# Performance work log

Hardware: AMD Instinct MI355X
Metric: run time of the kernel (lower is better)

## Reference

```python
import jax, jax.numpy as jnp
import numpy as np

NEG_SLOPE = 0.2


def gat_layer(x, W, a_src, a_dst, b, src, dst, num_nodes, heads, out_c, concat):
    # Linear transform per head: [N, heads, out_c]
    h = (x @ W).reshape(num_nodes, heads, out_c)
    # Per-node attention logits for source/dest roles: [N, heads]
    e_src = jnp.einsum('nhc,hc->nh', h, a_src)
    e_dst = jnp.einsum('nhc,hc->nh', h, a_dst)
    # Edge-wise scores (gather), LeakyReLU: [E, heads]
    e = jax.nn.leaky_relu(e_src[src] + e_dst[dst], negative_slope=NEG_SLOPE)
    # Segment softmax over incoming edges of each destination node
    m = jax.ops.segment_max(e, dst, num_segments=num_nodes)
    ex = jnp.exp(e - m[dst])
    denom = jax.ops.segment_sum(ex, dst, num_segments=num_nodes)
    alpha = ex / denom[dst]                       # [E, heads]
    # Weighted scatter-aggregate of source messages: [N, heads, out_c]
    out = jax.ops.segment_sum(h[src] * alpha[:, :, None], dst, num_segments=num_nodes)
    if concat:
        out = out.reshape(num_nodes, heads * out_c)
    else:
        out = out.mean(axis=1)
    return out + b


def setup_inputs() -> dict:
    key = jax.random.key(0)
    ks = jax.random.split(key, 12)
    N, E = 50000, 800000
    in_c, out_c, heads = 128, 32, 4
    x = jax.random.normal(ks[0], (N, in_c), dtype=jnp.float32)
    edge_index = jax.random.randint(ks[1], (2, E), 0, N, dtype=jnp.int64)
    s1 = 1.0 / np.sqrt(in_c)
    W1 = jax.random.normal(ks[2], (in_c, heads * out_c), dtype=jnp.float32) * s1
    a_src1 = jax.random.normal(ks[3], (heads, out_c), dtype=jnp.float32) * 0.1
    a_dst1 = jax.random.normal(ks[4], (heads, out_c), dtype=jnp.float32) * 0.1
    b1 = jnp.zeros((heads * out_c,), dtype=jnp.float32)
    s2 = 1.0 / np.sqrt(heads * out_c)
    W2 = jax.random.normal(ks[5], (heads * out_c, out_c), dtype=jnp.float32) * s2
    a_src2 = jax.random.normal(ks[6], (1, out_c), dtype=jnp.float32) * 0.1
    a_dst2 = jax.random.normal(ks[7], (1, out_c), dtype=jnp.float32) * 0.1
    b2 = jnp.zeros((out_c,), dtype=jnp.float32)
    return {"x": x, "edge_index": edge_index, "W1": W1, "a_src1": a_src1,
            "a_dst1": a_dst1, "b1": b1, "W2": W2, "a_src2": a_src2,
            "a_dst2": a_dst2, "b2": b2}


def reference(x, edge_index, W1, a_src1, a_dst1, b1, W2, a_src2, a_dst2, b2):
    N = x.shape[0]
    heads, out_c = a_src1.shape
    # add_self_loops=True (PyG default)
    loops = jnp.arange(N, dtype=edge_index.dtype)
    src = jnp.concatenate([edge_index[0], loops])
    dst = jnp.concatenate([edge_index[1], loops])
    h1 = gat_layer(x, W1, a_src1, a_dst1, b1, src, dst, N, heads, out_c, concat=True)
    h1 = jax.nn.elu(h1)
    out = gat_layer(h1, W2, a_src2, a_dst2, b2, src, dst, N, 1, out_c, concat=False)
    return out
```

## Files before the change

kernel.cpp:

```cpp
#include <hip/hip_runtime.h>
#include <hip/hip_bf16.h>

#define LRELU_SLOPE 0.2f
#define NB_SHIFT 7
#define NBLK 512

typedef __attribute__((ext_vector_type(8))) short short8;
typedef __attribute__((ext_vector_type(4))) float float4v;

__device__ inline float b2f(unsigned short u) {
    union { unsigned int i; float f; } v; v.i = ((unsigned int)u) << 16; return v.f;
}
__device__ inline unsigned short f2b(float f) {
    union { float f; unsigned int i; } v; v.f = f;
    unsigned int x = v.i;
    unsigned int r = x + 0x7fffu + ((x >> 16) & 1u);
    return (unsigned short)(r >> 16);
}
__device__ inline float lrelu(float x) { return x > 0.f ? x : LRELU_SLOPE * x; }

__global__ __launch_bounds__(256) void gemm1_mfma_kernel(
        const float* __restrict__ x, const float* __restrict__ W1,
        const float* __restrict__ a_src, const float* __restrict__ a_dst,
        unsigned short* __restrict__ h1b, float* __restrict__ es,
        float* __restrict__ ed, int N,
        const int* __restrict__ dst, int E, int Etot, int nb, int chunk,
        int* __restrict__ cnt) {
    __shared__ unsigned short xs[64][136];
    __shared__ unsigned short wt[128][136];
    int tid = threadIdx.x;
    int n0 = blockIdx.x * 64;

    for (int i = tid; i < 128 * 128; i += 256) {
        int k = i >> 7, n = i & 127;
        wt[n][k] = f2b(W1[i]);
    }
    for (int i = tid; i < 64 * 128; i += 256) {
        int r = i >> 7, k = i & 127;
        int row = n0 + r; if (row >= N) row = N - 1;
        xs[r][k] = f2b(x[(size_t)row * 128 + k]);
    }
    __syncthreads();

    int wave = tid >> 6;
    int lane = tid & 63;
    int lrow = lane & 15;
    int quad = lane >> 4;

    short8 afr[4];
#pragma unroll
    for (int kc = 0; kc < 4; kc++)
        afr[kc] = *(const short8*)&xs[wave * 16 + lrow][kc * 32 + quad * 8];
    __syncthreads();

#pragma unroll
    for (int ct = 0; ct < 8; ct++) {
        float4v acc = {0.f, 0.f, 0.f, 0.f};
#pragma unroll
        for (int kc = 0; kc < 4; kc++) {
            short8 bfr = *(const short8*)&wt[ct * 16 + lrow][kc * 32 + quad * 8];
            acc = __builtin_amdgcn_mfma_f32_16x16x32_bf16(afr[kc], bfr, acc, 0, 0, 0);
        }
#pragma unroll
        for (int r = 0; r < 4; r++) {
            int lr = wave * 16 + quad * 4 + r;
            int grow = n0 + lr;
            unsigned short hb = f2b(acc[r]);
            xs[lr][ct * 16 + lrow] = hb;
            if (grow < N)
                h1b[grow * 128 + ct * 16 + lrow] = hb;
        }
    }
    __syncthreads();

    int row = tid >> 2, h = tid & 3;
    int rg = n0 + row;
    if (rg < N) {
        const float* ap = a_src + h * 32;
        const float* bp = a_dst + h * 32;
        float s = 0.f, d = 0.f;
#pragma unroll
        for (int c2 = 0; c2 < 16; c2++) {
            unsigned int u = *(const unsigned int*)&xs[row][h * 32 + 2 * c2];
            float v0 = b2f((unsigned short)(u & 0xffffu));
            float v1 = b2f((unsigned short)(u >> 16));
            float2 a = *(const float2*)&ap[2 * c2];
            float2 b = *(const float2*)&bp[2 * c2];
            s += v0 * a.x + v1 * a.y;
            d += v0 * b.x + v1 * b.y;
        }
        es[rg * 4 + h] = s;
        ed[rg * 4 + h] = d;
    }

    int* histm = (int*)&wt[0][0];
    int blk = blockIdx.x;
    if (blk < NBLK)
        for (int i = tid; i < nb; i += 256) histm[i] = 0;
    __syncthreads();
    if (blk < NBLK) {
        int lo = blk * chunk;
        int hi = lo + chunk; if (hi > Etot) hi = Etot;
        for (int i = lo + tid; i < hi; i += 256) {
            int d = (i < E) ? dst[i] : (i - E);
            atomicAdd(&histm[d >> NB_SHIFT], 1);
        }
    }
    __syncthreads();
    if (blk < NBLK)
        for (int b = tid; b < nb; b += 256)
            cnt[b * NBLK + blk] = histm[b];
}

__global__ __launch_bounds__(1024) void scanA_kernel(int* cnt, int* bsum, int M) {
    __shared__ int tile[1024];
    int i = blockIdx.x * 1024 + threadIdx.x;
    int v = (i < M) ? cnt[i] : 0;
    tile[threadIdx.x] = v;
    __syncthreads();
    for (int off = 1; off < 1024; off <<= 1) {
        int t = (threadIdx.x >= (unsigned)off) ? tile[threadIdx.x - off] : 0;
        __syncthreads();
        tile[threadIdx.x] += t;
        __syncthreads();
    }
    int incl = tile[threadIdx.x];
    if (i < M) cnt[i] = incl - v;
    if (threadIdx.x == 1023) bsum[blockIdx.x] = incl;
}

__global__ __launch_bounds__(256) void scanB_kernel(int* __restrict__ bsum, int nb) {
    __shared__ int tile[256];
    int v = (threadIdx.x < (unsigned)nb) ? bsum[threadIdx.x] : 0;
    tile[threadIdx.x] = v;
    __syncthreads();
    for (int off = 1; off < 256; off <<= 1) {
        int t = (threadIdx.x >= (unsigned)off) ? tile[threadIdx.x - off] : 0;
        __syncthreads();
        tile[threadIdx.x] += t;
        __syncthreads();
    }
    if (threadIdx.x < (unsigned)nb) bsum[threadIdx.x] = tile[threadIdx.x] - v;
}

__global__ __launch_bounds__(256) void partition_kernel(
        const int* __restrict__ src, const int* __restrict__ dst,
        int E, int Etot, int nb, int chunk,
        const int* __restrict__ cnt, const int* __restrict__ boff,
        int2* __restrict__ bkt) {
    __shared__ int cur[512];
    int blk = blockIdx.x;
    for (int b = threadIdx.x; b < nb; b += 256) {
        int idx = b * NBLK + blk;
        cur[b] = cnt[idx] + boff[idx >> 10];
    }
    __syncthreads();
    int lo = blk * chunk;
    int hi = lo + chunk; if (hi > Etot) hi = Etot;
    for (int i = lo + threadIdx.x; i < hi; i += 256) {
        int s, d;
        if (i < E) { s = src[i]; d = dst[i]; }
        else       { s = d = i - E; }
        int pos = atomicAdd(&cur[d >> NB_SHIFT], 1);
        bkt[pos] = make_int2(s, d);
    }
}

__global__ __launch_bounds__(256) void finalize_kernel(
        const int2* __restrict__ bkt, const int* __restrict__ cnt,
        const int* __restrict__ boff, int nb,
        const float* __restrict__ es, const float* __restrict__ ed,
        int* __restrict__ ptr, int* __restrict__ csr_src,
        _Float16* __restrict__ w1h, int N, int Etot) {
    __shared__ int deg[128];
    __shared__ int scn[128];
    __shared__ int cur[128];
    int b = blockIdx.x;
    int idx0 = b * NBLK;
    int base = cnt[idx0] + boff[idx0 >> 10];
    int nextbase;
    if (b + 1 < nb) {
        int idx1 = (b + 1) * NBLK;
        nextbase = cnt[idx1] + boff[idx1 >> 10];
    } else nextbase = Etot;
    int count = nextbase - base;
    int node0 = b << NB_SHIFT;
    int nodes = N - node0; if (nodes > 128) nodes = 128;

    if (threadIdx.x < 128) deg[threadIdx.x] = 0;
    __syncthreads();
    for (int i = threadIdx.x; i < count; i += 256)
        atomicAdd(&deg[bkt[base + i].y - node0], 1);
    __syncthreads();
    int v = (threadIdx.x < 128) ? deg[threadIdx.x] : 0;
    if (threadIdx.x < 128) scn[threadIdx.x] = v;
    __syncthreads();
    for (int off = 1; off < 128; off <<= 1) {
        int t = (threadIdx.x < 128 && threadIdx.x >= (unsigned)off) ? scn[threadIdx.x - off] : 0;
        __syncthreads();
        if (threadIdx.x < 128) scn[threadIdx.x] += t;
        __syncthreads();
    }
    if (threadIdx.x < 128) {
        int excl = scn[threadIdx.x] - v;
        cur[threadIdx.x] = excl;
        if (threadIdx.x < nodes) ptr[node0 + threadIdx.x] = base + excl;
    }
    if (b == nb - 1 && threadIdx.x == 0) ptr[N] = Etot;
    __syncthreads();
    for (int i = threadIdx.x; i < count; i += 256) {
        int2 sd = bkt[base + i];
        int pos = base + atomicAdd(&cur[sd.y - node0], 1);
        csr_src[pos] = sd.x;
        float4 a = *(const float4*)&es[sd.x * 4];
        float4 bb = *(const float4*)&ed[sd.y * 4];
        union { _Float16 h[4]; uint2 u; } ww;
        ww.h[0] = (_Float16)__expf(lrelu(a.x + bb.x));
        ww.h[1] = (_Float16)__expf(lrelu(a.y + bb.y));
        ww.h[2] = (_Float16)__expf(lrelu(a.z + bb.z));
        ww.h[3] = (_Float16)__expf(lrelu(a.w + bb.w));
        *(uint2*)&w1h[(size_t)pos * 4] = ww.u;
    }
}

__global__ __launch_bounds__(256) void gemm2_mfma_kernel(
        const unsigned short* __restrict__ h1e, const float* __restrict__ W2,
        const float* __restrict__ a_src, const float* __restrict__ a_dst,
        unsigned short* __restrict__ h2b, float* __restrict__ es,
        float* __restrict__ ed, int N) {
    __shared__ unsigned short xs[64][136];
    __shared__ unsigned short wt[32][136];
    int tid = threadIdx.x;
    int n0 = blockIdx.x * 64;

    for (int i = tid; i < 128 * 32; i += 256) {
        int k = i >> 5, n = i & 31;
        wt[n][k] = f2b(W2[i]);
    }
    {
        const unsigned int* srcp = (const unsigned int*)(h1e + (size_t)n0 * 128);
        int rows = (N - n0) < 64 ? (N - n0) : 64;
        int maxu = rows * 64;
        for (int i = tid; i < 4096; i += 256) {
            unsigned int v = (i < maxu) ? srcp[i] : 0u;
            int r = i >> 6, cp = (i & 63) << 1;
            *(unsigned int*)&xs[r][cp] = v;
        }
    }
    __syncthreads();

    int wave = tid >> 6;
    int lane = tid & 63;
    int lrow = lane & 15;
    int quad = lane >> 4;

    short8 afr[4];
#pragma unroll
    for (int kc = 0; kc < 4; kc++)
        afr[kc] = *(const short8*)&xs[wave * 16 + lrow][kc * 32 + quad * 8];
    __syncthreads();

#pragma unroll
    for (int ct = 0; ct < 2; ct++) {
        float4v acc = {0.f, 0.f, 0.f, 0.f};
#pragma unroll
        for (int kc = 0; kc < 4; kc++) {
            short8 bfr = *(const short8*)&wt[ct * 16 + lrow][kc * 32 + quad * 8];
            acc = __builtin_amdgcn_mfma_f32_16x16x32_bf16(afr[kc], bfr, acc, 0, 0, 0);
        }
#pragma unroll
        for (int r = 0; r < 4; r++) {
            int lr = wave * 16 + quad * 4 + r;
            int grow = n0 + lr;
            unsigned short hb = f2b(acc[r]);
            xs[lr][ct * 16 + lrow] = hb;
            if (grow < N)
                h2b[(size_t)grow * 32 + ct * 16 + lrow] = hb;
        }
    }
    __syncthreads();

    if (tid < 64) {
        int rg = n0 + tid;
        if (rg < N) {
            float s = 0.f, d = 0.f;
#pragma unroll
            for (int c2 = 0; c2 < 16; c2++) {
                unsigned int u = *(const unsigned int*)&xs[tid][2 * c2];
                float v0 = b2f((unsigned short)(u & 0xffffu));
                float v1 = b2f((unsigned short)(u >> 16));
                float2 a = *(const float2*)&a_src[2 * c2];
                float2 b = *(const float2*)&a_dst[2 * c2];
                s += v0 * a.x + v1 * a.y;
                d += v0 * b.x + v1 * b.y;
            }
            es[rg] = s;
            ed[rg] = d;
        }
    }
}

__global__ __launch_bounds__(256) void agg1_kernel(
        const uint4* __restrict__ h1v, const _Float16* __restrict__ w1h,
        const int* __restrict__ csr, const int* __restrict__ ptr,
        const float* __restrict__ b1, uint4* __restrict__ h1e_v, int N) {
    int tid = threadIdx.x;
    int n = blockIdx.x * 16 + (tid >> 4);
    if (n >= N) return;
    int cl = tid & 15;
    int h = cl >> 2;
    int start = ptr[n], end = ptr[n + 1];
    float a0 = 0.f, a1 = 0.f, a2 = 0.f, a3 = 0.f;
    float a4 = 0.f, a5 = 0.f, a6 = 0.f, a7 = 0.f, ws = 0.f;
    int i = start;
    for (; i + 4 <= end; i += 4) {
        int s[4]; float v[4]; uint4 g[4];
#pragma unroll
        for (int k = 0; k < 4; k++) s[k] = csr[i + k];
#pragma unroll
        for (int k = 0; k < 4; k++) v[k] = (float)w1h[(size_t)(i + k) * 4 + h];
#pragma unroll
        for (int k = 0; k < 4; k++) g[k] = h1v[(s[k] << 4) + cl];
#pragma unroll
        for (int k = 0; k < 4; k++) {
            a0 += v[k] * b2f((unsigned short)(g[k].x & 0xffffu));
            a1 += v[k] * b2f((unsigned short)(g[k].x >> 16));
            a2 += v[k] * b2f((unsigned short)(g[k].y & 0xffffu));
            a3 += v[k] * b2f((unsigned short)(g[k].y >> 16));
            a4 += v[k] * b2f((unsigned short)(g[k].z & 0xffffu));
            a5 += v[k] * b2f((unsigned short)(g[k].z >> 16));
            a6 += v[k] * b2f((unsigned short)(g[k].w & 0xffffu));
            a7 += v[k] * b2f((unsigned short)(g[k].w >> 16));
            ws += v[k];
        }
    }
    for (; i < end; i++) {
        int s = csr[i];
        float v = (float)w1h[(size_t)i * 4 + h];
        uint4 g = h1v[(s << 4) + cl];
        a0 += v * b2f((unsigned short)(g.x & 0xffffu));
        a1 += v * b2f((unsigned short)(g.x >> 16));
        a2 += v * b2f((unsigned short)(g.y & 0xffffu));
        a3 += v * b2f((unsigned short)(g.y >> 16));
        a4 += v * b2f((unsigned short)(g.z & 0xffffu));
        a5 += v * b2f((unsigned short)(g.z >> 16));
        a6 += v * b2f((unsigned short)(g.w & 0xffffu));
        a7 += v * b2f((unsigned short)(g.w >> 16));
        ws += v;
    }
    float r = 1.f / ws;
    float4 bb0 = ((const float4*)b1)[cl * 2];
    float4 bb1 = ((const float4*)b1)[cl * 2 + 1];
    float o0 = a0 * r + bb0.x;
    float o1 = a1 * r + bb0.y;
    float o2 = a2 * r + bb0.z;
    float o3 = a3 * r + bb0.w;
    float o4 = a4 * r + bb1.x;
    float o5 = a5 * r + bb1.y;
    float o6 = a6 * r + bb1.z;
    float o7 = a7 * r + bb1.w;
    o0 = o0 > 0.f ? o0 : __expf(o0) - 1.f;
    o1 = o1 > 0.f ? o1 : __expf(o1) - 1.f;
    o2 = o2 > 0.f ? o2 : __expf(o2) - 1.f;
    o3 = o3 > 0.f ? o3 : __expf(o3) - 1.f;
    o4 = o4 > 0.f ? o4 : __expf(o4) - 1.f;
    o5 = o5 > 0.f ? o5 : __expf(o5) - 1.f;
    o6 = o6 > 0.f ? o6 : __expf(o6) - 1.f;
    o7 = o7 > 0.f ? o7 : __expf(o7) - 1.f;
    uint4 outv;
    outv.x = (unsigned int)f2b(o0) | ((unsigned int)f2b(o1) << 16);
    outv.y = (unsigned int)f2b(o2) | ((unsigned int)f2b(o3) << 16);
    outv.z = (unsigned int)f2b(o4) | ((unsigned int)f2b(o5) << 16);
    outv.w = (unsigned int)f2b(o6) | ((unsigned int)f2b(o7) << 16);
    h1e_v[(n << 4) + cl] = outv;
}

__global__ __launch_bounds__(256) void agg2_kernel(
        const uint2* __restrict__ h2v, const float* __restrict__ es,
        const float* __restrict__ ed, const int* __restrict__ csr,
        const int* __restrict__ ptr, const float* __restrict__ b2,
        float* __restrict__ out, int N) {
    int tid = threadIdx.x;
    int n = blockIdx.x * 32 + (tid >> 3);
    if (n >= N) return;
    int cl = tid & 7;
    float edl = ed[n];
    int start = ptr[n], end = ptr[n + 1];
    float a0 = 0.f, a1 = 0.f, a2 = 0.f, a3 = 0.f, ws = 0.f;
    int i = start;
    for (; i + 8 <= end; i += 8) {
        int s[8]; float e[8]; uint2 g[8];
#pragma unroll
        for (int k = 0; k < 8; k++) s[k] = csr[i + k];
#pragma unroll
        for (int k = 0; k < 8; k++) e[k] = es[s[k]];
#pragma unroll
        for (int k = 0; k < 8; k++) g[k] = h2v[(s[k] << 3) + cl];
#pragma unroll
        for (int k = 0; k < 8; k++) {
            float v = __expf(lrelu(e[k] + edl));
            a0 += v * b2f((unsigned short)(g[k].x & 0xffffu));
            a1 += v * b2f((unsigned short)(g[k].x >> 16));
            a2 += v * b2f((unsigned short)(g[k].y & 0xffffu));
            a3 += v * b2f((unsigned short)(g[k].y >> 16));
            ws += v;
        }
    }
    for (; i < end; i++) {
        int s = csr[i];
        float v = __expf(lrelu(es[s] + edl));
        uint2 g = h2v[(s << 3) + cl];
        a0 += v * b2f((unsigned short)(g.x & 0xffffu));
        a1 += v * b2f((unsigned short)(g.x >> 16));
        a2 += v * b2f((unsigned short)(g.y & 0xffffu));
        a3 += v * b2f((unsigned short)(g.y >> 16));
        ws += v;
    }
    float r = 1.f / ws;
    float4 bb = ((const float4*)b2)[cl];
    float4 o;
    o.x = a0 * r + bb.x;
    o.y = a1 * r + bb.y;
    o.z = a2 * r + bb.z;
    o.w = a3 * r + bb.w;
    ((float4*)out)[(size_t)n * 8 + cl] = o;
}

extern "C" void kernel_launch(void* const* d_in, const int* in_sizes, int n_in,
                              void* d_out, int out_size, void* d_ws, size_t ws_size,
                              hipStream_t stream) {
    const float* x      = (const float*)d_in[0];
    const int*   ei     = (const int*)  d_in[1];
    const float* W1     = (const float*)d_in[2];
    const float* a_src1 = (const float*)d_in[3];
    const float* a_dst1 = (const float*)d_in[4];
    const float* b1     = (const float*)d_in[5];
    const float* W2     = (const float*)d_in[6];
    const float* a_src2 = (const float*)d_in[7];
    const float* a_dst2 = (const float*)d_in[8];
    const float* b2     = (const float*)d_in[9];
    float* outp = (float*)d_out;

    const int N = in_sizes[0] / 128;
    const int E = in_sizes[1] / 2;
    const int Etot = E + N;

    const int* src = ei;
    const int* dst = ei + E;

    const int nb    = (N + 127) >> 7;
    const int chunk = (Etot + NBLK - 1) / NBLK;
    const int M = nb * NBLK;
    const int nbA = (M + 1023) / 1024;

    char* w = (char*)d_ws;
    unsigned short* h1b = (unsigned short*)(w + 0);
    unsigned short* h1e = (unsigned short*)(w + 12800000);
    unsigned short* h2b = (unsigned short*)(w + 25600000);
    float* es1  = (float*)(w + 28800000);
    float* ed1  = (float*)(w + 29600000);
    float* es2  = (float*)(w + 30400000);
    float* ed2  = (float*)(w + 30600000);
    int*   ptr  = (int*)  (w + 30800000);
    int*   bsum = (int*)  (w + 31000064);
    int*   cnt  = (int*)  (w + 31001088);
    int*   csr_src = (int*)(w + 31801856);
    int2*  bkt  = (int2*) (w + 35201856);
    _Float16* w1h = (_Float16*)(w + 42001856);

    gemm1_mfma_kernel<<<(N + 63) / 64, 256, 0, stream>>>(x, W1, a_src1, a_dst1,
                                                         h1b, es1, ed1, N,
                                                         dst, E, Etot, nb, chunk, cnt);

    scanA_kernel<<<nbA, 1024, 0, stream>>>(cnt, bsum, M);
    scanB_kernel<<<1, 256, 0, stream>>>(bsum, nbA);
    partition_kernel<<<NBLK, 256, 0, stream>>>(src, dst, E, Etot, nb, chunk,
                                               cnt, bsum, bkt);
    finalize_kernel<<<nb, 256, 0, stream>>>(bkt, cnt, bsum, nb, es1, ed1,
                                            ptr, csr_src, w1h, N, Etot);

    agg1_kernel<<<(N + 15) / 16, 256, 0, stream>>>((const uint4*)h1b, w1h,
                                                   csr_src, ptr, b1,
                                                   (uint4*)h1e, N);

    gemm2_mfma_kernel<<<(N + 63) / 64, 256, 0, stream>>>(h1e, W2, a_src2, a_dst2,
                                                         h2b, es2, ed2, N);
    agg2_kernel<<<(N + 31) / 32, 256, 0, stream>>>((const uint2*)h2b, es2, ed2,
                                                   csr_src, ptr, b2, outp, N);
}
```

Before: 198.6 us.

## Fuse scan kernels, recompute edge weights in aggregation, vectorize x load, halve partition blocks

Merges the two-level scan into one kernel, where the last block to finish (tracked by an atomic counter that gemm1 resets) scans the block sums. Edge attention weights are no longer precomputed and stored as fp16 in finalize. agg1 now gathers es per source and recomputes exp(leaky_relu) inline, which removes a per-edge buffer write and read at the cost of an extra gather and exp per lane. The x tile load in gemm1 becomes float4-vectorized, and the partition block count drops from 512 to 256, shrinking the count matrix and scan.

```diff
diff --git a/kernel.cpp b/kernel.cpp
--- a/kernel.cpp
+++ b/kernel.cpp
@@ -3,7 +3,7 @@
 
 #define LRELU_SLOPE 0.2f
 #define NB_SHIFT 7
-#define NBLK 512
+#define NBLK 256
 
 typedef __attribute__((ext_vector_type(8))) short short8;
 typedef __attribute__((ext_vector_type(4))) float float4v;
@@ -25,20 +25,29 @@
         unsigned short* __restrict__ h1b, float* __restrict__ es,
         float* __restrict__ ed, int N,
         const int* __restrict__ dst, int E, int Etot, int nb, int chunk,
-        int* __restrict__ cnt) {
+        int* __restrict__ cnt, int* __restrict__ done_ctr) {
     __shared__ unsigned short xs[64][136];
     __shared__ unsigned short wt[128][136];
     int tid = threadIdx.x;
     int n0 = blockIdx.x * 64;
+    if (blockIdx.x == 0 && tid == 0) done_ctr[0] = 0;
 
     for (int i = tid; i < 128 * 128; i += 256) {
         int k = i >> 7, n = i & 127;
         wt[n][k] = f2b(W1[i]);
     }
-    for (int i = tid; i < 64 * 128; i += 256) {
-        int r = i >> 7, k = i & 127;
-        int row = n0 + r; if (row >= N) row = N - 1;
-        xs[r][k] = f2b(x[(size_t)row * 128 + k]);
+    {
+        int rows = N - n0; if (rows > 64) rows = 64;
+        const float4* xv = (const float4*)(x + (size_t)n0 * 128);
+        int lim = rows * 32;
+        for (int i = tid; i < lim; i += 256) {
+            float4 v = xv[i];
+            int r = i >> 5, c4 = (i & 31) << 2;
+            uint2 p;
+            p.x = (unsigned int)f2b(v.x) | ((unsigned int)f2b(v.y) << 16);
+            p.y = (unsigned int)f2b(v.z) | ((unsigned int)f2b(v.w) << 16);
+            *(uint2*)&xs[r][c4] = p;
+        }
     }
     __syncthreads();
 
@@ -112,8 +121,10 @@
             cnt[b * NBLK + blk] = histm[b];
 }
 
-__global__ __launch_bounds__(1024) void scanA_kernel(int* cnt, int* bsum, int M) {
+__global__ __launch_bounds__(1024) void scanAB_kernel(int* cnt, int* bsum, int M,
+                                                      int nbA, int* done_ctr) {
     __shared__ int tile[1024];
+    __shared__ int amLast;
     int i = blockIdx.x * 1024 + threadIdx.x;
     int v = (i < M) ? cnt[i] : 0;
     tile[threadIdx.x] = v;
@@ -127,20 +138,22 @@
     int incl = tile[threadIdx.x];
     if (i < M) cnt[i] = incl - v;
     if (threadIdx.x == 1023) bsum[blockIdx.x] = incl;
-}
-
-__global__ __launch_bounds__(256) void scanB_kernel(int* __restrict__ bsum, int nb) {
-    __shared__ int tile[256];
-    int v = (threadIdx.x < (unsigned)nb) ? bsum[threadIdx.x] : 0;
-    tile[threadIdx.x] = v;
-    __syncthreads();
-    for (int off = 1; off < 256; off <<= 1) {
-        int t = (threadIdx.x >= (unsigned)off) ? tile[threadIdx.x - off] : 0;
+    __threadfence();
+    if (threadIdx.x == 0)
+        amLast = (atomicAdd(done_ctr, 1) == (int)gridDim.x - 1);
+    __syncthreads();
+    if (amLast) {
+        int vv = (threadIdx.x < (unsigned)nbA) ? bsum[threadIdx.x] : 0;
+        tile[threadIdx.x] = vv;
         __syncthreads();
-        tile[threadIdx.x] += t;
-        __syncthreads();
-    }
-    if (threadIdx.x < (unsigned)nb) bsum[threadIdx.x] = tile[threadIdx.x] - v;
+        for (int off = 1; off < 1024; off <<= 1) {
+            int t = (threadIdx.x >= (unsigned)off) ? tile[threadIdx.x - off] : 0;
+            __syncthreads();
+            tile[threadIdx.x] += t;
+            __syncthreads();
+        }
+        if (threadIdx.x < (unsigned)nbA) bsum[threadIdx.x] = tile[threadIdx.x] - vv;
+    }
 }
 
 __global__ __launch_bounds__(256) void partition_kernel(
@@ -169,9 +182,7 @@
 __global__ __launch_bounds__(256) void finalize_kernel(
         const int2* __restrict__ bkt, const int* __restrict__ cnt,
         const int* __restrict__ boff, int nb,
-        const float* __restrict__ es, const float* __restrict__ ed,
-        int* __restrict__ ptr, int* __restrict__ csr_src,
-        _Float16* __restrict__ w1h, int N, int Etot) {
+        int* __restrict__ ptr, int* __restrict__ csr_src, int N, int Etot) {
     __shared__ int deg[128];
     __shared__ int scn[128];
     __shared__ int cur[128];
@@ -212,14 +223,6 @@
         int2 sd = bkt[base + i];
         int pos = base + atomicAdd(&cur[sd.y - node0], 1);
         csr_src[pos] = sd.x;
-        float4 a = *(const float4*)&es[sd.x * 4];
-        float4 bb = *(const float4*)&ed[sd.y * 4];
-        union { _Float16 h[4]; uint2 u; } ww;
-        ww.h[0] = (_Float16)__expf(lrelu(a.x + bb.x));
-        ww.h[1] = (_Float16)__expf(lrelu(a.y + bb.y));
-        ww.h[2] = (_Float16)__expf(lrelu(a.z + bb.z));
-        ww.h[3] = (_Float16)__expf(lrelu(a.w + bb.w));
-        *(uint2*)&w1h[(size_t)pos * 4] = ww.u;
     }
 }
 
@@ -301,42 +304,45 @@
 }
 
 __global__ __launch_bounds__(256) void agg1_kernel(
-        const uint4* __restrict__ h1v, const _Float16* __restrict__ w1h,
-        const int* __restrict__ csr, const int* __restrict__ ptr,
-        const float* __restrict__ b1, uint4* __restrict__ h1e_v, int N) {
+        const uint4* __restrict__ h1v, const float* __restrict__ es,
+        const float* __restrict__ ed, const int* __restrict__ csr,
+        const int* __restrict__ ptr, const float* __restrict__ b1,
+        uint4* __restrict__ h1e_v, int N) {
     int tid = threadIdx.x;
     int n = blockIdx.x * 16 + (tid >> 4);
     if (n >= N) return;
     int cl = tid & 15;
     int h = cl >> 2;
+    float edl = ed[(n << 2) + h];
     int start = ptr[n], end = ptr[n + 1];
     float a0 = 0.f, a1 = 0.f, a2 = 0.f, a3 = 0.f;
     float a4 = 0.f, a5 = 0.f, a6 = 0.f, a7 = 0.f, ws = 0.f;
     int i = start;
     for (; i + 4 <= end; i += 4) {
-        int s[4]; float v[4]; uint4 g[4];
+        int s[4]; float e[4]; uint4 g[4];
 #pragma unroll
         for (int k = 0; k < 4; k++) s[k] = csr[i + k];
 #pragma unroll
-        for (int k = 0; k < 4; k++) v[k] = (float)w1h[(size_t)(i + k) * 4 + h];
+        for (int k = 0; k < 4; k++) e[k] = es[(s[k] << 2) + h];
 #pragma unroll
         for (int k = 0; k < 4; k++) g[k] = h1v[(s[k] << 4) + cl];
 #pragma unroll
         for (int k = 0; k < 4; k++) {
-            a0 += v[k] * b2f((unsigned short)(g[k].x & 0xffffu));
-            a1 += v[k] * b2f((unsigned short)(g[k].x >> 16));
-            a2 += v[k] * b2f((unsigned short)(g[k].y & 0xffffu));
-            a3 += v[k] * b2f((unsigned short)(g[k].y >> 16));
-            a4 += v[k] * b2f((unsigned short)(g[k].z & 0xffffu));
-            a5 += v[k] * b2f((unsigned short)(g[k].z >> 16));
-            a6 += v[k] * b2f((unsigned short)(g[k].w & 0xffffu));
-            a7 += v[k] * b2f((unsigned short)(g[k].w >> 16));
-            ws += v[k];
+            float v = __expf(lrelu(e[k] + edl));
+            a0 += v * b2f((unsigned short)(g[k].x & 0xffffu));
+            a1 += v * b2f((unsigned short)(g[k].x >> 16));
+            a2 += v * b2f((unsigned short)(g[k].y & 0xffffu));
+            a3 += v * b2f((unsigned short)(g[k].y >> 16));
+            a4 += v * b2f((unsigned short)(g[k].z & 0xffffu));
+            a5 += v * b2f((unsigned short)(g[k].z >> 16));
+            a6 += v * b2f((unsigned short)(g[k].w & 0xffffu));
+            a7 += v * b2f((unsigned short)(g[k].w >> 16));
+            ws += v;
         }
     }
     for (; i < end; i++) {
         int s = csr[i];
-        float v = (float)w1h[(size_t)i * 4 + h];
+        float v = __expf(lrelu(es[(s << 2) + h] + edl));
         uint4 g = h1v[(s << 4) + cl];
         a0 += v * b2f((unsigned short)(g.x & 0xffffu));
         a1 += v * b2f((unsigned short)(g.x >> 16));
@@ -463,23 +469,23 @@
     float* ed2  = (float*)(w + 30600000);
     int*   ptr  = (int*)  (w + 30800000);
     int*   bsum = (int*)  (w + 31000064);
-    int*   cnt  = (int*)  (w + 31001088);
-    int*   csr_src = (int*)(w + 31801856);
-    int2*  bkt  = (int2*) (w + 35201856);
-    _Float16* w1h = (_Float16*)(w + 42001856);
+    int*   done = (int*)  (w + 31001088);
+    int*   cnt  = (int*)  (w + 31001152);
+    int*   csr_src = (int*)(w + 31401536);
+    int2*  bkt  = (int2*) (w + 34801536);
 
     gemm1_mfma_kernel<<<(N + 63) / 64, 256, 0, stream>>>(x, W1, a_src1, a_dst1,
                                                          h1b, es1, ed1, N,
-                                                         dst, E, Etot, nb, chunk, cnt);
-
-    scanA_kernel<<<nbA, 1024, 0, stream>>>(cnt, bsum, M);
-    scanB_kernel<<<1, 256, 0, stream>>>(bsum, nbA);
+                                                         dst, E, Etot, nb, chunk,
+                                                         cnt, done);
+
+    scanAB_kernel<<<nbA, 1024, 0, stream>>>(cnt, bsum, M, nbA, done);
     partition_kernel<<<NBLK, 256, 0, stream>>>(src, dst, E, Etot, nb, chunk,
                                                cnt, bsum, bkt);
-    finalize_kernel<<<nb, 256, 0, stream>>>(bkt, cnt, bsum, nb, es1, ed1,
-                                            ptr, csr_src, w1h, N, Etot);
-
-    agg1_kernel<<<(N + 15) / 16, 256, 0, stream>>>((const uint4*)h1b, w1h,
+    finalize_kernel<<<nb, 256, 0, stream>>>(bkt, cnt, bsum, nb, ptr, csr_src,
+                                            N, Etot);
+
+    agg1_kernel<<<(N + 15) / 16, 256, 0, stream>>>((const uint4*)h1b, es1, ed1,
                                                    csr_src, ptr, b1,
                                                    (uint4*)h1e, N);
 
```

New measurement: 217.7 us. +9.6%, slower.
